# Kernel optimization log

Measured on AMD Instinct MI355X. Metric: run time of the kernel, lower is better.

The kernel has to match this reference:

```python
import jax, jax.numpy as jnp
from jax import lax
import numpy as np

HIDDEN = 256

def _lstm_layer(x_tbf, w_ih, w_hh, b_ih, b_hh):
    # x_tbf: [T, B, F]; w_ih: [4H, F]; w_hh: [4H, H]
    B = x_tbf.shape[1]
    # precompute input projections for all timesteps: [T, B, 4H]
    xg = jnp.einsum('tbf,gf->tbg', x_tbf, w_ih) + b_ih + b_hh
    def step(carry, xg_t):
        h, c = carry
        g = xg_t + h @ w_hh.T  # [B, 4H]
        i, f, gg, o = jnp.split(g, 4, axis=-1)  # torch gate order: i, f, g, o
        i = jax.nn.sigmoid(i)
        f = jax.nn.sigmoid(f)
        gg = jnp.tanh(gg)
        o = jax.nn.sigmoid(o)
        c = f * c + i * gg
        h = o * jnp.tanh(c)
        return (h, c), h
    init = (jnp.zeros((B, HIDDEN), x_tbf.dtype), jnp.zeros((B, HIDDEN), x_tbf.dtype))
    _, hs = lax.scan(step, init, xg)
    return hs  # [T, B, H]


def setup_inputs() -> dict:
    key = jax.random.key(0)
    ks = jax.random.split(key, 16)
    B, T, F_IN, NSPK = 64, 1024, 40, 1251
    s = 1.0 / np.sqrt(HIDDEN)
    def u(k, shape):
        return jax.random.uniform(k, shape, jnp.float32, -s, s)
    inp = {'x': jax.random.normal(ks[0], (B, T, F_IN), jnp.float32)}
    in_dims = [F_IN, HIDDEN, HIDDEN]
    ki = 1
    for l in range(3):
        inp[f'w_ih{l}'] = u(ks[ki], (4 * HIDDEN, in_dims[l])); ki += 1
        inp[f'w_hh{l}'] = u(ks[ki], (4 * HIDDEN, HIDDEN)); ki += 1
        inp[f'b_ih{l}'] = u(ks[ki], (4 * HIDDEN,)); ki += 1
        inp[f'b_hh{l}'] = u(ks[ki], (4 * HIDDEN,)); ki += 1
    inp['w_lin'] = u(ks[13], (NSPK, HIDDEN))
    inp['b_lin'] = u(ks[14], (NSPK,))
    return inp


def reference(x, w_ih0, w_hh0, b_ih0, b_hh0, w_ih1, w_hh1, b_ih1, b_hh1,
              w_ih2, w_hh2, b_ih2, b_hh2, w_lin, b_lin):
    # x: [B, T, F] (batch_first). Run 3 stacked LSTM layers.
    h = jnp.transpose(x, (1, 0, 2))  # [T, B, F]
    params = [(w_ih0, w_hh0, b_ih0, b_hh0),
              (w_ih1, w_hh1, b_ih1, b_hh1),
              (w_ih2, w_hh2, b_ih2, b_hh2)]
    for w_ih, w_hh, b_ih, b_hh in params:
        h = _lstm_layer(h, w_ih, w_hh, b_ih, b_hh)
    lstm_out = jnp.transpose(h, (1, 0, 2))  # [B, T, H]
    # Faithful to original: lstm_out[-1] selects the LAST BATCH element -> [T, H]
    last = lstm_out[-1]
    logits = last @ w_lin.T + b_lin  # [T, NSPK]
    return jax.nn.log_softmax(logits, axis=1)
```

## Files before the change

### kernel.cpp

```cpp
#include <hip/hip_runtime.h>

#define HID 256
#define T_STEPS 1024
#define F_IN 40
#define NSPK 1251
#define NCHUNK 8
#define NBLOCKS 64
#define K2_THREADS 512

#define HBUF_WORDS (3 * 1025 * 256)
#define H2F_OFF_BYTES ((size_t)HBUF_WORDS * 8)

__device__ __forceinline__ float fast_sig(float v) {
    return __builtin_amdgcn_rcpf(1.f + __expf(-v));
}
__device__ __forceinline__ float fast_tanh(float v) {
    return 2.f * __builtin_amdgcn_rcpf(1.f + __expf(-2.f * v)) - 1.f;
}

__device__ __forceinline__ float poll_word(const unsigned long long* p, unsigned want) {
    unsigned long long v0 = __hip_atomic_load(p, __ATOMIC_RELAXED, __HIP_MEMORY_SCOPE_AGENT);
    if ((unsigned)(v0 >> 32) == want) return __uint_as_float((unsigned)v0);
    unsigned long long v1 = __hip_atomic_load(p, __ATOMIC_RELAXED, __HIP_MEMORY_SCOPE_AGENT);
    unsigned long long v2 = __hip_atomic_load(p, __ATOMIC_RELAXED, __HIP_MEMORY_SCOPE_AGENT);
    unsigned long long v3 = __hip_atomic_load(p, __ATOMIC_RELAXED, __HIP_MEMORY_SCOPE_AGENT);
    for (;;) {
        if ((unsigned)(v0 >> 32) == want) return __uint_as_float((unsigned)v0);
        v0 = v1; v1 = v2; v2 = v3;
        v3 = __hip_atomic_load(p, __ATOMIC_RELAXED, __HIP_MEMORY_SCOPE_AGENT);
    }
}

__global__ void k0_init(unsigned long long* __restrict__ hbuf) {
    int tid = threadIdx.x;
    if (tid < 3 * HID) {
        int l = tid / HID, k = tid % HID;
        hbuf[(size_t)(l * 1025 + 0) * HID + k] = 0ull;
    }
}

__global__ __launch_bounds__(K2_THREADS) void k2_lstm(
    const float* __restrict__ x,
    const float* __restrict__ w_ih0, const float* __restrict__ w_hh0,
    const float* __restrict__ b_ih0, const float* __restrict__ b_hh0,
    const float* __restrict__ w_ih1, const float* __restrict__ w_hh1,
    const float* __restrict__ b_ih1, const float* __restrict__ b_hh1,
    const float* __restrict__ w_ih2, const float* __restrict__ w_hh2,
    const float* __restrict__ b_ih2, const float* __restrict__ b_hh2,
    unsigned long long* __restrict__ hbuf, float* __restrict__ h2f)
{
    const int bid = blockIdx.x;
    const int xslot = bid & 7;
    if (xslot >= 3) return;
    const int layer = xslot;
    const int g     = bid >> 3;
    const int tid   = threadIdx.x;
    const int seg = tid & 15;
    const int j   = tid >> 4;
    const int jg  = g * 32 + j;

    const float* wih = (layer == 0) ? w_ih0 : (layer == 1) ? w_ih1 : w_ih2;
    const float* whh = (layer == 0) ? w_hh0 : (layer == 1) ? w_hh1 : w_hh2;
    const float* bih = (layer == 0) ? b_ih0 : (layer == 1) ? b_ih1 : b_ih2;
    const float* bhh = (layer == 0) ? b_hh0 : (layer == 1) ? b_hh1 : b_hh2;

    __shared__ float buf[512];
    __shared__ float hv_lds[32];

    float w[4][32];
    float bb[4];
    const int rot = (2 * seg) & 31;
    #pragma unroll
    for (int q = 0; q < 4; q++) {
        const int r = q * 256 + jg;
        bb[q] = bih[r] + bhh[r];
        if (layer > 0) {
            #pragma unroll
            for (int i = 0; i < 32; i++) {
                int k = seg * 32 + ((i + rot) & 31);
                w[q][i] = (k < HID) ? wih[(size_t)r * HID + k]
                                    : whh[(size_t)r * HID + (k - HID)];
            }
        } else {
            #pragma unroll
            for (int i = 0; i < 32; i++) {
                int k = seg * 32 + ((i + rot) & 31);
                w[q][i] = (k < F_IN) ? w_ih0[r * F_IN + k]
                        : (k >= HID) ? whh[(size_t)r * HID + (k - HID)]
                                     : 0.f;
            }
        }
    }

    for (int i = tid; i < 512; i += K2_THREADS) buf[i] = 0.f;
    if (tid < 32) hv_lds[tid] = 0.f;
    __syncthreads();

    const float* x63 = x + 63 * T_STEPS * F_IN;
    const unsigned long long* h_prev_layer = hbuf + (size_t)(layer - 1) * 1025 * HID;
    unsigned long long* h_own              = hbuf + (size_t)layer * 1025 * HID;

    float4 px = make_float4(0.f, 0.f, 0.f, 0.f);
    if (layer == 0 && tid >= 256 && tid < 256 + 10)
        px = ((const float4*)x63)[tid - 256];

    float c_state = 0.f;

    for (int t = 0; t < T_STEPS; t++) {
        if (tid < 256) {
            if ((tid >> 5) == g) {
                buf[256 + tid] = hv_lds[tid & 31];
            } else {
                buf[256 + tid] = poll_word(h_own + (size_t)t * HID + tid, (unsigned)t);
            }
        } else if (layer > 0) {
            buf[tid - 256] = poll_word(h_prev_layer + (size_t)(t + 1) * HID + (tid - 256),
                                       (unsigned)(t + 1));
        } else if (tid < 256 + 10) {
            ((float4*)buf)[tid - 256] = px;
            if (t + 1 < T_STEPS)
                px = ((const float4*)(x63 + (t + 1) * F_IN))[tid - 256];
        }
        __syncthreads();

        float a0 = 0.f, a1 = 0.f, a2 = 0.f, a3 = 0.f;
        const float* bufs = buf + seg * 32;
        #pragma unroll
        for (int i = 0; i < 32; i++) {
            float f = bufs[(i + rot) & 31];
            a0 += w[0][i] * f;
            a1 += w[1][i] * f;
            a2 += w[2][i] * f;
            a3 += w[3][i] * f;
        }
        #pragma unroll
        for (int m = 1; m < 16; m <<= 1) {
            a0 += __shfl_xor(a0, m, 64);
            a1 += __shfl_xor(a1, m, 64);
            a2 += __shfl_xor(a2, m, 64);
            a3 += __shfl_xor(a3, m, 64);
        }

        if (seg == 0) {
            float si = fast_sig(a0 + bb[0]);
            float sf = fast_sig(a1 + bb[1]);
            float gg = fast_tanh(a2 + bb[2]);
            float so = fast_sig(a3 + bb[3]);
            c_state = sf * c_state + si * gg;
            float hv = so * fast_tanh(c_state);
            hv_lds[j] = hv;
        }
        __syncthreads();

        if (tid < 32) {
            float hv = hv_lds[tid];
            unsigned long long word =
                ((unsigned long long)(unsigned)(t + 1) << 32) | (unsigned long long)__float_as_uint(hv);
            __hip_atomic_store(h_own + (size_t)(t + 1) * HID + g * 32 + tid, word,
                               __ATOMIC_RELAXED, __HIP_MEMORY_SCOPE_AGENT);
            if (layer == 2) h2f[(size_t)t * HID + g * 32 + tid] = hv;
        }
    }
}

#define BM 64
#define BN 64
#define BK 32
__global__ __launch_bounds__(256) void k3_logits(
    const float* __restrict__ A, const float* __restrict__ w_lin,
    const float* __restrict__ b_lin, float* __restrict__ out)
{
    int m0 = blockIdx.x * BM;
    int n0 = blockIdx.y * BN;
    int tid = threadIdx.x;
    __shared__ float As[BM][BK + 1];
    __shared__ float Bs[BN][BK + 1];
    float accv[4][4] = {};
    int tx = tid % 16, ty = tid / 16;

    for (int k0 = 0; k0 < HID; k0 += BK) {
        int row = tid / 4;
        int kq  = (tid % 4) * 8;
        {
            const float4* src = (const float4*)(A + (m0 + row) * HID + k0 + kq);
            float4 v0 = src[0], v1 = src[1];
            As[row][kq + 0] = v0.x; As[row][kq + 1] = v0.y; As[row][kq + 2] = v0.z; As[row][kq + 3] = v0.w;
            As[row][kq + 4] = v1.x; As[row][kq + 5] = v1.y; As[row][kq + 6] = v1.z; As[row][kq + 7] = v1.w;
        }
        {
            int n = n0 + row;
            float4 v0 = make_float4(0.f, 0.f, 0.f, 0.f), v1 = v0;
            if (n < NSPK) {
                const float4* src = (const float4*)(w_lin + n * HID + k0 + kq);
                v0 = src[0]; v1 = src[1];
            }
            Bs[row][kq + 0] = v0.x; Bs[row][kq + 1] = v0.y; Bs[row][kq + 2] = v0.z; Bs[row][kq + 3] = v0.w;
            Bs[row][kq + 4] = v1.x; Bs[row][kq + 5] = v1.y; Bs[row][kq + 6] = v1.z; Bs[row][kq + 7] = v1.w;
        }
        __syncthreads();
        #pragma unroll
        for (int kk = 0; kk < BK; kk++) {
            float a0 = As[ty * 4 + 0][kk], a1 = As[ty * 4 + 1][kk];
            float a2 = As[ty * 4 + 2][kk], a3 = As[ty * 4 + 3][kk];
            float b0 = Bs[tx * 4 + 0][kk], b1 = Bs[tx * 4 + 1][kk];
            float b2 = Bs[tx * 4 + 2][kk], b3 = Bs[tx * 4 + 3][kk];
            accv[0][0] += a0 * b0; accv[0][1] += a0 * b1; accv[0][2] += a0 * b2; accv[0][3] += a0 * b3;
            accv[1][0] += a1 * b0; accv[1][1] += a1 * b1; accv[1][2] += a1 * b2; accv[1][3] += a1 * b3;
            accv[2][0] += a2 * b0; accv[2][1] += a2 * b1; accv[2][2] += a2 * b2; accv[2][3] += a2 * b3;
            accv[3][0] += a3 * b0; accv[3][1] += a3 * b1; accv[3][2] += a3 * b2; accv[3][3] += a3 * b3;
        }
        __syncthreads();
    }
    #pragma unroll
    for (int i = 0; i < 4; i++) {
        int m = m0 + ty * 4 + i;
        #pragma unroll
        for (int j = 0; j < 4; j++) {
            int n = n0 + tx * 4 + j;
            if (n < NSPK) out[(size_t)m * NSPK + n] = accv[i][j] + b_lin[n];
        }
    }
}

__global__ __launch_bounds__(256) void k4_logsoftmax(float* __restrict__ out)
{
    int t = blockIdx.x;
    float* row = out + (size_t)t * NSPK;
    int tid = threadIdx.x;
    __shared__ float red[8];
    float vals[5];
    float lmax = -1e30f;
    #pragma unroll
    for (int k = 0; k < 5; k++) {
        int n = tid + k * 256;
        vals[k] = (n < NSPK) ? row[n] : -1e30f;
        lmax = fmaxf(lmax, vals[k]);
    }
    #pragma unroll
    for (int m = 1; m < 64; m <<= 1) lmax = fmaxf(lmax, __shfl_xor(lmax, m, 64));
    int wave = tid >> 6;
    if ((tid & 63) == 0) red[wave] = lmax;
    __syncthreads();
    float gmax = fmaxf(fmaxf(red[0], red[1]), fmaxf(red[2], red[3]));
    float lsum = 0.f;
    #pragma unroll
    for (int k = 0; k < 5; k++) {
        int n = tid + k * 256;
        if (n < NSPK) lsum += __expf(vals[k] - gmax);
    }
    #pragma unroll
    for (int m = 1; m < 64; m <<= 1) lsum += __shfl_xor(lsum, m, 64);
    if ((tid & 63) == 0) red[4 + wave] = lsum;
    __syncthreads();
    float lse = logf(red[4] + red[5] + red[6] + red[7]) + gmax;
    #pragma unroll
    for (int k = 0; k < 5; k++) {
        int n = tid + k * 256;
        if (n < NSPK) row[n] = vals[k] - lse;
    }
}

extern "C" void kernel_launch(void* const* d_in, const int* in_sizes, int n_in,
                              void* d_out, int out_size, void* d_ws, size_t ws_size,
                              hipStream_t stream) {
    const float* x     = (const float*)d_in[0];
    const float* w_ih0 = (const float*)d_in[1];
    const float* w_hh0 = (const float*)d_in[2];
    const float* b_ih0 = (const float*)d_in[3];
    const float* b_hh0 = (const float*)d_in[4];
    const float* w_ih1 = (const float*)d_in[5];
    const float* w_hh1 = (const float*)d_in[6];
    const float* b_ih1 = (const float*)d_in[7];
    const float* b_hh1 = (const float*)d_in[8];
    const float* w_ih2 = (const float*)d_in[9];
    const float* w_hh2 = (const float*)d_in[10];
    const float* b_ih2 = (const float*)d_in[11];
    const float* b_hh2 = (const float*)d_in[12];
    const float* w_lin = (const float*)d_in[13];
    const float* b_lin = (const float*)d_in[14];

    unsigned long long* hbuf = (unsigned long long*)d_ws;
    float* h2f = (float*)((char*)d_ws + H2F_OFF_BYTES);
    float* out = (float*)d_out;

    k0_init<<<1, 1024, 0, stream>>>(hbuf);
    k2_lstm<<<NBLOCKS, K2_THREADS, 0, stream>>>(
        x, w_ih0, w_hh0, b_ih0, b_hh0,
        w_ih1, w_hh1, b_ih1, b_hh1,
        w_ih2, w_hh2, b_ih2, b_hh2,
        hbuf, h2f);
    k3_logits<<<dim3(16, 20), 256, 0, stream>>>(h2f, w_lin, b_lin, out);
    k4_logsoftmax<<<T_STEPS, 256, 0, stream>>>(out);
}
```

Baseline: 1.864 ms.

## Restructure LSTM step to one barrier per timestep with cross-wave gate reduction

Changes the thread mapping so each wavefront holds two 32-wide input segments for all 32 hidden units. Partial sums go through a double-buffered LDS gate buffer, and one lane group finishes the reduction and the activation. This removes the second __syncthreads per timestep and the 16-way shuffle reduction, and loads weights with float4. Dead waves in layer 0 skip the unused input segments. Each block now polls its own hidden values from global memory instead of taking them from LDS, and correctness depends on the s_waitcnt-only ordering between the LDS buffer writes and the reads that follow.

```diff
diff --git a/kernel.cpp b/kernel.cpp
--- a/kernel.cpp
+++ b/kernel.cpp
@@ -55,8 +55,9 @@
     const int layer = xslot;
     const int g     = bid >> 3;
     const int tid   = threadIdx.x;
-    const int seg = tid & 15;
-    const int j   = tid >> 4;
+    const int seg = tid >> 5;
+    const int j   = tid & 31;
+    const int wv  = tid >> 6;
     const int jg  = g * 32 + j;
 
     const float* wih = (layer == 0) ? w_ih0 : (layer == 1) ? w_ih1 : w_ih2;
@@ -64,96 +65,115 @@
     const float* bih = (layer == 0) ? b_ih0 : (layer == 1) ? b_ih1 : b_ih2;
     const float* bhh = (layer == 0) ? b_hh0 : (layer == 1) ? b_hh1 : b_hh2;
 
-    __shared__ float buf[512];
-    __shared__ float hv_lds[32];
+    const bool dead = (layer == 0) && (seg >= 2) && (seg < 8);
+
+    __shared__ float  buf[512];
+    __shared__ float4 gatebuf[2][8][32];
 
     float w[4][32];
     float bb[4];
-    const int rot = (2 * seg) & 31;
-    #pragma unroll
-    for (int q = 0; q < 4; q++) {
-        const int r = q * 256 + jg;
-        bb[q] = bih[r] + bhh[r];
-        if (layer > 0) {
+    if (!dead) {
+        #pragma unroll
+        for (int q = 0; q < 4; q++) {
+            const int r = q * 256 + jg;
+            bb[q] = bih[r] + bhh[r];
+            const int k0 = seg * 32;
+            if (k0 >= 256) {
+                const float4* src = (const float4*)(whh + (size_t)r * HID + (k0 - 256));
+                #pragma unroll
+                for (int i4 = 0; i4 < 8; i4++) {
+                    float4 v = src[i4];
+                    w[q][i4*4+0] = v.x; w[q][i4*4+1] = v.y;
+                    w[q][i4*4+2] = v.z; w[q][i4*4+3] = v.w;
+                }
+            } else if (layer > 0) {
+                const float4* src = (const float4*)(wih + (size_t)r * HID + k0);
+                #pragma unroll
+                for (int i4 = 0; i4 < 8; i4++) {
+                    float4 v = src[i4];
+                    w[q][i4*4+0] = v.x; w[q][i4*4+1] = v.y;
+                    w[q][i4*4+2] = v.z; w[q][i4*4+3] = v.w;
+                }
+            } else {
+                #pragma unroll
+                for (int i = 0; i < 32; i++) {
+                    int k = k0 + i;
+                    w[q][i] = (k < F_IN) ? w_ih0[r * F_IN + k] : 0.f;
+                }
+            }
+        }
+    } else {
+        #pragma unroll
+        for (int q = 0; q < 4; q++) {
+            bb[q] = 0.f;
             #pragma unroll
-            for (int i = 0; i < 32; i++) {
-                int k = seg * 32 + ((i + rot) & 31);
-                w[q][i] = (k < HID) ? wih[(size_t)r * HID + k]
-                                    : whh[(size_t)r * HID + (k - HID)];
-            }
-        } else {
+            for (int i = 0; i < 32; i++) w[q][i] = 0.f;
+        }
+    }
+
+    for (int i = tid; i < 512; i += K2_THREADS) buf[i] = 0.f;
+    __syncthreads();
+
+    const float* x63 = x + 63 * T_STEPS * F_IN;
+    const unsigned long long* h_prev = hbuf + (size_t)(layer - 1) * 1025 * HID;
+    unsigned long long* h_own        = hbuf + (size_t)layer * 1025 * HID;
+
+    float px = 0.f;
+    if (layer == 0 && tid < F_IN) px = x63[tid];
+
+    float c_state = 0.f;
+
+    for (int t = 0; t < T_STEPS; t++) {
+        if (!dead) {
+            if (tid < 256) {
+                if (layer > 0) {
+                    buf[tid] = poll_word(h_prev + (size_t)(t + 1) * HID + tid,
+                                         (unsigned)(t + 1));
+                } else if (tid < F_IN) {
+                    buf[tid] = px;
+                    if (t + 1 < T_STEPS) px = x63[(t + 1) * F_IN + tid];
+                }
+            } else {
+                buf[tid] = poll_word(h_own + (size_t)t * HID + (tid - 256),
+                                     (unsigned)t);
+            }
+        }
+
+        float4 part = make_float4(0.f, 0.f, 0.f, 0.f);
+        if (!dead) {
+            __asm__ volatile("s_waitcnt lgkmcnt(0)" ::: "memory");
+            const float4* b4 = (const float4*)buf + seg * 8;
+            float a0 = 0.f, a1 = 0.f, a2 = 0.f, a3 = 0.f;
             #pragma unroll
-            for (int i = 0; i < 32; i++) {
-                int k = seg * 32 + ((i + rot) & 31);
-                w[q][i] = (k < F_IN) ? w_ih0[r * F_IN + k]
-                        : (k >= HID) ? whh[(size_t)r * HID + (k - HID)]
-                                     : 0.f;
-            }
-        }
-    }
-
-    for (int i = tid; i < 512; i += K2_THREADS) buf[i] = 0.f;
-    if (tid < 32) hv_lds[tid] = 0.f;
-    __syncthreads();
-
-    const float* x63 = x + 63 * T_STEPS * F_IN;
-    const unsigned long long* h_prev_layer = hbuf + (size_t)(layer - 1) * 1025 * HID;
-    unsigned long long* h_own              = hbuf + (size_t)layer * 1025 * HID;
-
-    float4 px = make_float4(0.f, 0.f, 0.f, 0.f);
-    if (layer == 0 && tid >= 256 && tid < 256 + 10)
-        px = ((const float4*)x63)[tid - 256];
-
-    float c_state = 0.f;
-
-    for (int t = 0; t < T_STEPS; t++) {
-        if (tid < 256) {
-            if ((tid >> 5) == g) {
-                buf[256 + tid] = hv_lds[tid & 31];
-            } else {
-                buf[256 + tid] = poll_word(h_own + (size_t)t * HID + tid, (unsigned)t);
-            }
-        } else if (layer > 0) {
-            buf[tid - 256] = poll_word(h_prev_layer + (size_t)(t + 1) * HID + (tid - 256),
-                                       (unsigned)(t + 1));
-        } else if (tid < 256 + 10) {
-            ((float4*)buf)[tid - 256] = px;
-            if (t + 1 < T_STEPS)
-                px = ((const float4*)(x63 + (t + 1) * F_IN))[tid - 256];
-        }
+            for (int i4 = 0; i4 < 8; i4++) {
+                float4 f = b4[i4];
+                a0 += w[0][i4*4+0]*f.x + w[0][i4*4+1]*f.y + w[0][i4*4+2]*f.z + w[0][i4*4+3]*f.w;
+                a1 += w[1][i4*4+0]*f.x + w[1][i4*4+1]*f.y + w[1][i4*4+2]*f.z + w[1][i4*4+3]*f.w;
+                a2 += w[2][i4*4+0]*f.x + w[2][i4*4+1]*f.y + w[2][i4*4+2]*f.z + w[2][i4*4+3]*f.w;
+                a3 += w[3][i4*4+0]*f.x + w[3][i4*4+1]*f.y + w[3][i4*4+2]*f.z + w[3][i4*4+3]*f.w;
+            }
+            a0 += __shfl_xor(a0, 32, 64);
+            a1 += __shfl_xor(a1, 32, 64);
+            a2 += __shfl_xor(a2, 32, 64);
+            a3 += __shfl_xor(a3, 32, 64);
+            part = make_float4(a0, a1, a2, a3);
+        }
+        if ((tid & 32) == 0) gatebuf[t & 1][wv][j] = part;
         __syncthreads();
 
-        float a0 = 0.f, a1 = 0.f, a2 = 0.f, a3 = 0.f;
-        const float* bufs = buf + seg * 32;
-        #pragma unroll
-        for (int i = 0; i < 32; i++) {
-            float f = bufs[(i + rot) & 31];
-            a0 += w[0][i] * f;
-            a1 += w[1][i] * f;
-            a2 += w[2][i] * f;
-            a3 += w[3][i] * f;
-        }
-        #pragma unroll
-        for (int m = 1; m < 16; m <<= 1) {
-            a0 += __shfl_xor(a0, m, 64);
-            a1 += __shfl_xor(a1, m, 64);
-            a2 += __shfl_xor(a2, m, 64);
-            a3 += __shfl_xor(a3, m, 64);
-        }
-
-        if (seg == 0) {
-            float si = fast_sig(a0 + bb[0]);
-            float sf = fast_sig(a1 + bb[1]);
-            float gg = fast_tanh(a2 + bb[2]);
-            float so = fast_sig(a3 + bb[3]);
+        if (tid < 32) {
+            float4 s = gatebuf[t & 1][0][tid];
+            #pragma unroll
+            for (int w8 = 1; w8 < 8; w8++) {
+                float4 v = gatebuf[t & 1][w8][tid];
+                s.x += v.x; s.y += v.y; s.z += v.z; s.w += v.w;
+            }
+            float si = fast_sig(s.x + bb[0]);
+            float sf = fast_sig(s.y + bb[1]);
+            float gg = fast_tanh(s.z + bb[2]);
+            float so = fast_sig(s.w + bb[3]);
             c_state = sf * c_state + si * gg;
             float hv = so * fast_tanh(c_state);
-            hv_lds[j] = hv;
-        }
-        __syncthreads();
-
-        if (tid < 32) {
-            float hv = hv_lds[tid];
             unsigned long long word =
                 ((unsigned long long)(unsigned)(t + 1) << 32) | (unsigned long long)__float_as_uint(hv);
             __hip_atomic_store(h_own + (size_t)(t + 1) * HID + g * 32 + tid, word,
```

After: 1.625 ms, median of 2. 1.15x faster.

## Double-buffer LSTM step buffer to drop second barrier and publish h directly

Applied to the files above, without the earlier changes.

The per-step LDS input buffer is now double-buffered, so each block's own h values go straight into the next step's buffer. This removes the second __syncthreads and the hv_lds staging per timestep. Each lane with sub==0 publishes its h value to global memory immediately instead of a separate group of 32 threads doing it after a barrier. The dot product now reads float4 from LDS with a rotated index to reduce bank conflicts, and the polling work is split differently between thread halves. The intent is to shorten the serial per-timestep critical path; the risk is a race on buffer reuse between steps.

```diff
diff --git a/kernel.cpp b/kernel.cpp
--- a/kernel.cpp
+++ b/kernel.cpp
@@ -18,7 +18,7 @@
     return 2.f * __builtin_amdgcn_rcpf(1.f + __expf(-2.f * v)) - 1.f;
 }
 
-__device__ __forceinline__ float poll_word(const unsigned long long* p, unsigned want) {
+__device__ __forceinline__ float poll_agent(const unsigned long long* p, unsigned want) {
     unsigned long long v0 = __hip_atomic_load(p, __ATOMIC_RELAXED, __HIP_MEMORY_SCOPE_AGENT);
     if ((unsigned)(v0 >> 32) == want) return __uint_as_float((unsigned)v0);
     unsigned long long v1 = __hip_atomic_load(p, __ATOMIC_RELAXED, __HIP_MEMORY_SCOPE_AGENT);
@@ -55,83 +55,79 @@
     const int layer = xslot;
     const int g     = bid >> 3;
     const int tid   = threadIdx.x;
-    const int seg = tid & 15;
-    const int j   = tid >> 4;
-    const int jg  = g * 32 + j;
+    const int lane  = tid & 63;
+    const int wv    = tid >> 6;
+    const int j_loc = lane >> 4;
+    const int sub   = lane & 15;
+    const int jg    = g * 32 + wv * 4 + j_loc;
 
     const float* wih = (layer == 0) ? w_ih0 : (layer == 1) ? w_ih1 : w_ih2;
     const float* whh = (layer == 0) ? w_hh0 : (layer == 1) ? w_hh1 : w_hh2;
     const float* bih = (layer == 0) ? b_ih0 : (layer == 1) ? b_ih1 : b_ih2;
     const float* bhh = (layer == 0) ? b_hh0 : (layer == 1) ? b_hh1 : b_hh2;
 
-    __shared__ float buf[512];
-    __shared__ float hv_lds[32];
+    __shared__ float buf[2][512];
 
     float w[4][32];
     float bb[4];
-    const int rot = (2 * seg) & 31;
     #pragma unroll
     for (int q = 0; q < 4; q++) {
         const int r = q * 256 + jg;
         bb[q] = bih[r] + bhh[r];
-        if (layer > 0) {
+        #pragma unroll
+        for (int i4 = 0; i4 < 8; i4++) {
+            const int kb = (i4 + sub) & 7;
             #pragma unroll
-            for (int i = 0; i < 32; i++) {
-                int k = seg * 32 + ((i + rot) & 31);
-                w[q][i] = (k < HID) ? wih[(size_t)r * HID + k]
-                                    : whh[(size_t)r * HID + (k - HID)];
+            for (int c = 0; c < 4; c++) {
+                const int k = 32 * sub + kb * 4 + c;
+                float wv_;
+                if (k >= 256)            wv_ = whh[(size_t)r * HID + (k - 256)];
+                else if (layer > 0)      wv_ = wih[(size_t)r * HID + k];
+                else                     wv_ = (k < F_IN) ? w_ih0[r * F_IN + k] : 0.f;
+                w[q][i4 * 4 + c] = wv_;
+            }
+        }
+    }
+
+    for (int i = tid; i < 1024; i += K2_THREADS) ((float*)buf)[i] = 0.f;
+    __syncthreads();
+
+    const float* x63 = x + 63 * T_STEPS * F_IN;
+    const unsigned long long* h_prev = hbuf + (size_t)(layer - 1) * 1025 * HID;
+    unsigned long long* h_own        = hbuf + (size_t)layer * 1025 * HID;
+
+    float px = 0.f;
+    if (layer == 0 && tid < F_IN) px = x63[tid];
+
+    float c_state = 0.f;
+
+    for (int t = 0; t < T_STEPS; t++) {
+        float* bp = buf[t & 1];
+
+        if (tid < 256) {
+            if (layer > 0) {
+                bp[tid] = poll_agent(h_prev + (size_t)(t + 1) * HID + tid, (unsigned)(t + 1));
+            } else if (tid < F_IN) {
+                bp[tid] = px;
+                if (t + 1 < T_STEPS) px = x63[(t + 1) * F_IN + tid];
             }
         } else {
-            #pragma unroll
-            for (int i = 0; i < 32; i++) {
-                int k = seg * 32 + ((i + rot) & 31);
-                w[q][i] = (k < F_IN) ? w_ih0[r * F_IN + k]
-                        : (k >= HID) ? whh[(size_t)r * HID + (k - HID)]
-                                     : 0.f;
-            }
-        }
-    }
-
-    for (int i = tid; i < 512; i += K2_THREADS) buf[i] = 0.f;
-    if (tid < 32) hv_lds[tid] = 0.f;
-    __syncthreads();
-
-    const float* x63 = x + 63 * T_STEPS * F_IN;
-    const unsigned long long* h_prev_layer = hbuf + (size_t)(layer - 1) * 1025 * HID;
-    unsigned long long* h_own              = hbuf + (size_t)layer * 1025 * HID;
-
-    float4 px = make_float4(0.f, 0.f, 0.f, 0.f);
-    if (layer == 0 && tid >= 256 && tid < 256 + 10)
-        px = ((const float4*)x63)[tid - 256];
-
-    float c_state = 0.f;
-
-    for (int t = 0; t < T_STEPS; t++) {
-        if (tid < 256) {
-            if ((tid >> 5) == g) {
-                buf[256 + tid] = hv_lds[tid & 31];
-            } else {
-                buf[256 + tid] = poll_word(h_own + (size_t)t * HID + tid, (unsigned)t);
-            }
-        } else if (layer > 0) {
-            buf[tid - 256] = poll_word(h_prev_layer + (size_t)(t + 1) * HID + (tid - 256),
-                                       (unsigned)(t + 1));
-        } else if (tid < 256 + 10) {
-            ((float4*)buf)[tid - 256] = px;
-            if (t + 1 < T_STEPS)
-                px = ((const float4*)(x63 + (t + 1) * F_IN))[tid - 256];
+            const int k = tid - 256;
+            if ((k >> 5) != g) {
+                bp[256 + k] = poll_agent(h_own + (size_t)t * HID + k, (unsigned)t);
+            }
         }
         __syncthreads();
 
         float a0 = 0.f, a1 = 0.f, a2 = 0.f, a3 = 0.f;
-        const float* bufs = buf + seg * 32;
-        #pragma unroll
-        for (int i = 0; i < 32; i++) {
-            float f = bufs[(i + rot) & 31];
-            a0 += w[0][i] * f;
-            a1 += w[1][i] * f;
-            a2 += w[2][i] * f;
-            a3 += w[3][i] * f;
+        const float4* b4 = (const float4*)bp + sub * 8;
+        #pragma unroll
+        for (int i4 = 0; i4 < 8; i4++) {
+            float4 f = b4[(i4 + sub) & 7];
+            a0 += w[0][i4*4+0]*f.x + w[0][i4*4+1]*f.y + w[0][i4*4+2]*f.z + w[0][i4*4+3]*f.w;
+            a1 += w[1][i4*4+0]*f.x + w[1][i4*4+1]*f.y + w[1][i4*4+2]*f.z + w[1][i4*4+3]*f.w;
+            a2 += w[2][i4*4+0]*f.x + w[2][i4*4+1]*f.y + w[2][i4*4+2]*f.z + w[2][i4*4+3]*f.w;
+            a3 += w[3][i4*4+0]*f.x + w[3][i4*4+1]*f.y + w[3][i4*4+2]*f.z + w[3][i4*4+3]*f.w;
         }
         #pragma unroll
         for (int m = 1; m < 16; m <<= 1) {
@@ -141,24 +137,20 @@
             a3 += __shfl_xor(a3, m, 64);
         }
 
-        if (seg == 0) {
-            float si = fast_sig(a0 + bb[0]);
-            float sf = fast_sig(a1 + bb[1]);
-            float gg = fast_tanh(a2 + bb[2]);
-            float so = fast_sig(a3 + bb[3]);
-            c_state = sf * c_state + si * gg;
-            float hv = so * fast_tanh(c_state);
-            hv_lds[j] = hv;
-        }
-        __syncthreads();
-
-        if (tid < 32) {
-            float hv = hv_lds[tid];
+        float si = fast_sig(a0 + bb[0]);
+        float sf = fast_sig(a1 + bb[1]);
+        float gg = fast_tanh(a2 + bb[2]);
+        float so = fast_sig(a3 + bb[3]);
+        c_state = sf * c_state + si * gg;
+        float hv = so * fast_tanh(c_state);
+
+        if (sub == 0) {
+            buf[(t + 1) & 1][256 + jg] = hv;
             unsigned long long word =
                 ((unsigned long long)(unsigned)(t + 1) << 32) | (unsigned long long)__float_as_uint(hv);
-            __hip_atomic_store(h_own + (size_t)(t + 1) * HID + g * 32 + tid, word,
+            __hip_atomic_store(h_own + (size_t)(t + 1) * HID + jg, word,
                                __ATOMIC_RELAXED, __HIP_MEMORY_SCOPE_AGENT);
-            if (layer == 2) h2f[(size_t)t * HID + g * 32 + tid] = hv;
+            if (layer == 2) h2f[(size_t)t * HID + jg] = hv;
         }
     }
 }
```

After: 2.119 ms. 13.7% more time.
